# Kernel tuning notes

Measured on AMD Instinct MI355X. Metric: run time of the kernel, lower is better.

The kernel has to match this reference:

```python
import jax, jax.numpy as jnp
import numpy as np

NEG_INF = -1e18  # fp32 masking constant used by the original module


def setup_inputs() -> dict:
    key0 = jax.random.key(0)
    kq, kk, kv, km, ke = jax.random.split(key0, 5)
    B, L, H, C = 2, 2048, 16, 64
    query = jax.random.normal(kq, (B, L, H, C), dtype=jnp.float32)
    key = jax.random.normal(kk, (B, L, H, C), dtype=jnp.float32)
    value = jax.random.normal(kv, (B, L, H, C), dtype=jnp.float32)
    mask = jax.random.randint(km, (B, L, L), 0, 2).astype(jnp.bool_)
    edge_scores = jax.random.normal(ke, (1, H, L, L), dtype=jnp.float32)
    return {"query": query, "key": key, "value": value, "mask": mask,
            "edge_scores": edge_scores}


def _masked_softmax(att_score, mask):
    # mask: True -> keep, False -> masked. Fill with -1e18 (fp32 path),
    # softmax, then multiply by mask (post-softmax zeroing), as in original.
    s = jnp.where(mask, att_score, NEG_INF)
    w = jax.nn.softmax(s, axis=-1)
    return w * mask.astype(w.dtype)


def reference(query, key, value, mask, edge_scores):
    # layout 'NTK': query/key/value (B, L, H, C); mask (B, Lq, Lm)
    scale = jnp.sqrt(jnp.asarray(query.shape[-1], dtype=query.dtype))
    # scores: (B, H, Lq, Lm)
    scores = jnp.einsum('binc,bjnc->bnij', query, key)
    scores = scores + edge_scores
    attn_weights = _masked_softmax(scores / scale, mask[:, None, :, :])
    # dropout rate is 0.0 -> identity
    # context: (B, Lq, H, Cv) -> (B, Lq, H*Cv)
    context = jnp.einsum('bnij,bjnc->binc', attn_weights, value)
    B, Lq = context.shape[0], context.shape[1]
    context_vec = context.reshape(B, Lq, -1)
    return (context_vec, scores, attn_weights)
```

## Files before the change

kernel.cpp:

```cpp
#include <hip/hip_runtime.h>


typedef __attribute__((ext_vector_type(8))) short bf16x8;
typedef __attribute__((ext_vector_type(4))) float f32x4;

#define LQ 2048
#define NH 16
#define CD 64

__device__ inline short f2bf(float x) {
    union { float f; unsigned u; } v; v.f = x;
    unsigned r = v.u + 0x7FFFu + ((v.u >> 16) & 1u);
    return (short)(r >> 16);
}

__device__ inline bf16x8 pack8(float4 a, float4 b) {
    bf16x8 r;
    r[0] = f2bf(a.x); r[1] = f2bf(a.y); r[2] = f2bf(a.z); r[3] = f2bf(a.w);
    r[4] = f2bf(b.x); r[5] = f2bf(b.y); r[6] = f2bf(b.z); r[7] = f2bf(b.w);
    return r;
}

__global__ __launch_bounds__(256)
void k_stats(const float* __restrict__ q, const float* __restrict__ kk,
             const float* __restrict__ edge, const int* __restrict__ mask,
             float* __restrict__ lsum)
{
    __shared__ short Ks[64][72];
    __shared__ float Sf[4][16][68];
    const int z = blockIdx.y;
    const int b = z & 1, h = z >> 1;
    const int i0 = blockIdx.x * 64;
    const int tid = threadIdx.x;
    const int r = tid >> 2, seg = (tid & 3) * 16;
    const int wave = tid >> 6, lane = tid & 63;
    const int quad = lane >> 4, mm = lane & 15;

    const float* qp = q + ((size_t)((b * LQ + i0 + wave * 16 + mm) * NH + h)) * CD;
    float4 q0 = *(const float4*)(qp + quad * 8);
    float4 q1 = *(const float4*)(qp + quad * 8 + 4);
    float4 q2 = *(const float4*)(qp + 32 + quad * 8);
    float4 q3 = *(const float4*)(qp + 32 + quad * 8 + 4);
    bf16x8 a0 = pack8(q0, q1), a1 = pack8(q2, q3);

    float lacc[4] = {0.f, 0.f, 0.f, 0.f};

    for (int jb = 0; jb < 32; ++jb) {
        const int j0 = jb * 64;
        __syncthreads();
        const float* krow = kk + ((size_t)((b * LQ + j0 + r) * NH + h)) * CD + seg;
        #pragma unroll
        for (int u = 0; u < 4; ++u) {
            float4 g = ((const float4*)krow)[u];
            *(short4*)&Ks[r][seg + u * 4] = make_short4(f2bf(g.x), f2bf(g.y), f2bf(g.z), f2bf(g.w));
        }
        __syncthreads();

        #pragma unroll
        for (int jt = 0; jt < 4; ++jt) {
            bf16x8 b0 = *(const bf16x8*)&Ks[jt * 16 + mm][quad * 8];
            bf16x8 b1 = *(const bf16x8*)&Ks[jt * 16 + mm][32 + quad * 8];
            f32x4 a = {0.f, 0.f, 0.f, 0.f};
            a = __builtin_amdgcn_mfma_f32_16x16x32_bf16(a0, b0, a, 0, 0, 0);
            a = __builtin_amdgcn_mfma_f32_16x16x32_bf16(a1, b1, a, 0, 0, 0);
            #pragma unroll
            for (int reg = 0; reg < 4; ++reg)
                Sf[wave][quad * 4 + reg][jt * 16 + mm] = a[reg];
        }

        #pragma unroll
        for (int s = 0; s < 4; ++s) {
            const int rl = quad + 4 * s;
            const int gi = i0 + wave * 16 + rl;
            const int gj = j0 + mm * 4;
            float4 sv = *(const float4*)&Sf[wave][rl][mm * 4];
            float4 ev = *(const float4*)(edge + ((size_t)(h * LQ + gi)) * LQ + gj);
            int4   mv = *(const int4*)(mask + ((size_t)(b * LQ + gi)) * LQ + gj);
            float p0 = mv.x ? __expf((sv.x + ev.x) * 0.125f) : 0.f;
            float p1 = mv.y ? __expf((sv.y + ev.y) * 0.125f) : 0.f;
            float p2 = mv.z ? __expf((sv.z + ev.z) * 0.125f) : 0.f;
            float p3 = mv.w ? __expf((sv.w + ev.w) * 0.125f) : 0.f;
            lacc[s] += (p0 + p1) + (p2 + p3);
        }
    }

    #pragma unroll
    for (int s = 0; s < 4; ++s) {
        float v = lacc[s];
        #pragma unroll
        for (int o = 1; o <= 8; o <<= 1) v += __shfl_xor(v, o, 64);
        if (mm == 0)
            lsum[(size_t)(b * NH + h) * LQ + i0 + wave * 16 + quad + 4 * s] = v;
    }
}

__global__ __launch_bounds__(256)
void k_fused(const float* __restrict__ q, const float* __restrict__ kk,
             const float* __restrict__ v, const int* __restrict__ mask,
             const float* __restrict__ edge, const float* __restrict__ lsum,
             float* __restrict__ sc, float* __restrict__ attn,
             float* __restrict__ ctx)
{
    __shared__ short Ks[64][72];
    __shared__ short Vt[64][72];
    __shared__ float Sf[4][16][68];
    __shared__ short Wt[4][16][72];

    const int z = blockIdx.y;
    const int b = z & 1, h = z >> 1;
    const int i0 = blockIdx.x * 64;
    const int tid = threadIdx.x;
    const int r = tid >> 2, seg = (tid & 3) * 16;
    const int wave = tid >> 6, lane = tid & 63;
    const int quad = lane >> 4, mm = lane & 15;

    const float* qp = q + ((size_t)((b * LQ + i0 + wave * 16 + mm) * NH + h)) * CD;
    float4 q0 = *(const float4*)(qp + quad * 8);
    float4 q1 = *(const float4*)(qp + quad * 8 + 4);
    float4 q2 = *(const float4*)(qp + 32 + quad * 8);
    float4 q3 = *(const float4*)(qp + 32 + quad * 8 + 4);
    bf16x8 a0 = pack8(q0, q1), a1 = pack8(q2, q3);

    float inv[4];
    #pragma unroll
    for (int s = 0; s < 4; ++s) {
        float l = lsum[(size_t)(b * NH + h) * LQ + i0 + wave * 16 + quad + 4 * s];
        inv[s] = (l > 0.f) ? 1.f / l : 0.f;
    }

    f32x4 cacc[4] = { {0,0,0,0}, {0,0,0,0}, {0,0,0,0}, {0,0,0,0} };

    for (int jb = 0; jb < 32; ++jb) {
        const int j0 = jb * 64;
        __syncthreads();
        const float* krow = kk + ((size_t)((b * LQ + j0 + r) * NH + h)) * CD + seg;
        const float* vrow = v  + ((size_t)((b * LQ + j0 + r) * NH + h)) * CD + seg;
        #pragma unroll
        for (int u = 0; u < 4; ++u) {
            float4 g = ((const float4*)krow)[u];
            *(short4*)&Ks[r][seg + u * 4] = make_short4(f2bf(g.x), f2bf(g.y), f2bf(g.z), f2bf(g.w));
            float4 w = ((const float4*)vrow)[u];
            Vt[seg + u * 4 + 0][r] = f2bf(w.x);
            Vt[seg + u * 4 + 1][r] = f2bf(w.y);
            Vt[seg + u * 4 + 2][r] = f2bf(w.z);
            Vt[seg + u * 4 + 3][r] = f2bf(w.w);
        }
        __syncthreads();

        #pragma unroll
        for (int jt = 0; jt < 4; ++jt) {
            bf16x8 b0 = *(const bf16x8*)&Ks[jt * 16 + mm][quad * 8];
            bf16x8 b1 = *(const bf16x8*)&Ks[jt * 16 + mm][32 + quad * 8];
            f32x4 a = {0.f, 0.f, 0.f, 0.f};
            a = __builtin_amdgcn_mfma_f32_16x16x32_bf16(a0, b0, a, 0, 0, 0);
            a = __builtin_amdgcn_mfma_f32_16x16x32_bf16(a1, b1, a, 0, 0, 0);
            #pragma unroll
            for (int reg = 0; reg < 4; ++reg)
                Sf[wave][quad * 4 + reg][jt * 16 + mm] = a[reg];
        }

        #pragma unroll
        for (int s = 0; s < 4; ++s) {
            const int rl = quad + 4 * s;
            const int gi = i0 + wave * 16 + rl;
            const int gj = j0 + mm * 4;
            float4 sv = *(const float4*)&Sf[wave][rl][mm * 4];
            float4 ev = *(const float4*)(edge + ((size_t)(h * LQ + gi)) * LQ + gj);
            float4 s4 = make_float4(sv.x + ev.x, sv.y + ev.y, sv.z + ev.z, sv.w + ev.w);
            const size_t sidx = ((size_t)((b * NH + h) * LQ + gi)) * LQ + gj;
            *(float4*)(sc + sidx) = s4;
            int4 mv = *(const int4*)(mask + ((size_t)(b * LQ + gi)) * LQ + gj);
            const float iv = inv[s];
            float w0 = mv.x ? __expf(s4.x * 0.125f) * iv : 0.f;
            float w1 = mv.y ? __expf(s4.y * 0.125f) * iv : 0.f;
            float w2 = mv.z ? __expf(s4.z * 0.125f) * iv : 0.f;
            float w3 = mv.w ? __expf(s4.w * 0.125f) * iv : 0.f;
            *(float4*)(attn + sidx) = make_float4(w0, w1, w2, w3);
            *(short4*)&Wt[wave][rl][mm * 4] = make_short4(f2bf(w0), f2bf(w1), f2bf(w2), f2bf(w3));
        }

        #pragma unroll
        for (int kt = 0; kt < 2; ++kt) {
            bf16x8 aw = *(const bf16x8*)&Wt[wave][mm][kt * 32 + quad * 8];
            #pragma unroll
            for (int nt = 0; nt < 4; ++nt) {
                bf16x8 bb = *(const bf16x8*)&Vt[nt * 16 + mm][kt * 32 + quad * 8];
                cacc[nt] = __builtin_amdgcn_mfma_f32_16x16x32_bf16(aw, bb, cacc[nt], 0, 0, 0);
            }
        }
    }

    const int irow = i0 + wave * 16 + quad * 4;
    #pragma unroll
    for (int nt = 0; nt < 4; ++nt) {
        const int c = nt * 16 + mm;
        #pragma unroll
        for (int reg = 0; reg < 4; ++reg) {
            const int i = irow + reg;
            ctx[((size_t)(b * LQ + i)) * (NH * CD) + h * CD + c] = cacc[nt][reg];
        }
    }
}

extern "C" void kernel_launch(void* const* d_in, const int* in_sizes, int n_in,
                              void* d_out, int out_size, void* d_ws, size_t ws_size,
                              hipStream_t stream) {
    const float* q    = (const float*)d_in[0];
    const float* k    = (const float*)d_in[1];
    const float* v    = (const float*)d_in[2];
    const int*   mask = (const int*)d_in[3];
    const float* edge = (const float*)d_in[4];

    float* out = (float*)d_out;
    float* ctx = out;
    float* sc  = out + 4194304;
    float* at  = sc + 134217728;

    float* lsum = (float*)d_ws;

    k_stats<<<dim3(32, 32), 256, 0, stream>>>(q, k, edge, mask, lsum);
    k_fused<<<dim3(32, 32), 256, 0, stream>>>(q, k, v, mask, edge, lsum, sc, at, ctx);
}
```

Before: 1.795 ms.

## Swap MFMA operands to drop LDS score staging and prefetch edge/mask tiles

Both kernels now compute S^T via swapped MFMA operands, so each lane holds four consecutive key columns of one query row in registers. This removes the Sf shared-memory round trip and its extra LDS traffic. Edge and mask values for the next key block are loaded into registers one iteration early to hide global latency. Launch bounds now request 4 blocks per CU, which may force register spills given the added prefetch registers.

```diff
diff --git a/kernel.cpp b/kernel.cpp
--- a/kernel.cpp
+++ b/kernel.cpp
@@ -21,13 +21,12 @@
     return r;
 }
 
-__global__ __launch_bounds__(256)
+__global__ __launch_bounds__(256, 4)
 void k_stats(const float* __restrict__ q, const float* __restrict__ kk,
              const float* __restrict__ edge, const int* __restrict__ mask,
              float* __restrict__ lsum)
 {
     __shared__ short Ks[64][72];
-    __shared__ float Sf[4][16][68];
     const int z = blockIdx.y;
     const int b = z & 1, h = z >> 1;
     const int i0 = blockIdx.x * 64;
@@ -36,14 +35,22 @@
     const int wave = tid >> 6, lane = tid & 63;
     const int quad = lane >> 4, mm = lane & 15;
 
-    const float* qp = q + ((size_t)((b * LQ + i0 + wave * 16 + mm) * NH + h)) * CD;
-    float4 q0 = *(const float4*)(qp + quad * 8);
-    float4 q1 = *(const float4*)(qp + quad * 8 + 4);
-    float4 q2 = *(const float4*)(qp + 32 + quad * 8);
-    float4 q3 = *(const float4*)(qp + 32 + quad * 8 + 4);
-    bf16x8 a0 = pack8(q0, q1), a1 = pack8(q2, q3);
-
-    float lacc[4] = {0.f, 0.f, 0.f, 0.f};
+    const int gi = i0 + wave * 16 + mm;
+    const float* qp = q + ((size_t)((b * LQ + gi) * NH + h)) * CD;
+    bf16x8 qa0 = pack8(*(const float4*)(qp + quad * 8), *(const float4*)(qp + quad * 8 + 4));
+    bf16x8 qa1 = pack8(*(const float4*)(qp + 32 + quad * 8), *(const float4*)(qp + 32 + quad * 8 + 4));
+
+    const float* erow = edge + ((size_t)(h * LQ + gi)) * LQ;
+    const int*   mrow = mask + ((size_t)(b * LQ + gi)) * LQ;
+
+    float4 ev[4]; int4 mv[4];
+    #pragma unroll
+    for (int jt = 0; jt < 4; ++jt) {
+        ev[jt] = *(const float4*)(erow + jt * 16 + quad * 4);
+        mv[jt] = *(const int4*)(mrow + jt * 16 + quad * 4);
+    }
+
+    float lacc = 0.f;
 
     for (int jb = 0; jb < 32; ++jb) {
         const int j0 = jb * 64;
@@ -56,45 +63,42 @@
         }
         __syncthreads();
 
-        #pragma unroll
-        for (int jt = 0; jt < 4; ++jt) {
-            bf16x8 b0 = *(const bf16x8*)&Ks[jt * 16 + mm][quad * 8];
-            bf16x8 b1 = *(const bf16x8*)&Ks[jt * 16 + mm][32 + quad * 8];
+        f32x4 acc[4];
+        #pragma unroll
+        for (int jt = 0; jt < 4; ++jt) {
+            bf16x8 k0 = *(const bf16x8*)&Ks[jt * 16 + mm][quad * 8];
+            bf16x8 k1 = *(const bf16x8*)&Ks[jt * 16 + mm][32 + quad * 8];
             f32x4 a = {0.f, 0.f, 0.f, 0.f};
-            a = __builtin_amdgcn_mfma_f32_16x16x32_bf16(a0, b0, a, 0, 0, 0);
-            a = __builtin_amdgcn_mfma_f32_16x16x32_bf16(a1, b1, a, 0, 0, 0);
+            a = __builtin_amdgcn_mfma_f32_16x16x32_bf16(k0, qa0, a, 0, 0, 0);
+            a = __builtin_amdgcn_mfma_f32_16x16x32_bf16(k1, qa1, a, 0, 0, 0);
+            acc[jt] = a;
+        }
+
+        #pragma unroll
+        for (int jt = 0; jt < 4; ++jt) {
+            float p0 = mv[jt].x ? __expf((acc[jt][0] + ev[jt].x) * 0.125f) : 0.f;
+            float p1 = mv[jt].y ? __expf((acc[jt][1] + ev[jt].y) * 0.125f) : 0.f;
+            float p2 = mv[jt].z ? __expf((acc[jt][2] + ev[jt].z) * 0.125f) : 0.f;
+            float p3 = mv[jt].w ? __expf((acc[jt][3] + ev[jt].w) * 0.125f) : 0.f;
+            lacc += (p0 + p1) + (p2 + p3);
+        }
+
+        if (jb < 31) {
             #pragma unroll
-            for (int reg = 0; reg < 4; ++reg)
-                Sf[wave][quad * 4 + reg][jt * 16 + mm] = a[reg];
-        }
-
-        #pragma unroll
-        for (int s = 0; s < 4; ++s) {
-            const int rl = quad + 4 * s;
-            const int gi = i0 + wave * 16 + rl;
-            const int gj = j0 + mm * 4;
-            float4 sv = *(const float4*)&Sf[wave][rl][mm * 4];
-            float4 ev = *(const float4*)(edge + ((size_t)(h * LQ + gi)) * LQ + gj);
-            int4   mv = *(const int4*)(mask + ((size_t)(b * LQ + gi)) * LQ + gj);
-            float p0 = mv.x ? __expf((sv.x + ev.x) * 0.125f) : 0.f;
-            float p1 = mv.y ? __expf((sv.y + ev.y) * 0.125f) : 0.f;
-            float p2 = mv.z ? __expf((sv.z + ev.z) * 0.125f) : 0.f;
-            float p3 = mv.w ? __expf((sv.w + ev.w) * 0.125f) : 0.f;
-            lacc[s] += (p0 + p1) + (p2 + p3);
-        }
-    }
-
-    #pragma unroll
-    for (int s = 0; s < 4; ++s) {
-        float v = lacc[s];
-        #pragma unroll
-        for (int o = 1; o <= 8; o <<= 1) v += __shfl_xor(v, o, 64);
-        if (mm == 0)
-            lsum[(size_t)(b * NH + h) * LQ + i0 + wave * 16 + quad + 4 * s] = v;
-    }
-}
-
-__global__ __launch_bounds__(256)
+            for (int jt = 0; jt < 4; ++jt) {
+                ev[jt] = *(const float4*)(erow + j0 + 64 + jt * 16 + quad * 4);
+                mv[jt] = *(const int4*)(mrow + j0 + 64 + jt * 16 + quad * 4);
+            }
+        }
+    }
+
+    lacc += __shfl_xor(lacc, 16, 64);
+    lacc += __shfl_xor(lacc, 32, 64);
+    if (quad == 0)
+        lsum[(size_t)(b * NH + h) * LQ + gi] = lacc;
+}
+
+__global__ __launch_bounds__(256, 4)
 void k_fused(const float* __restrict__ q, const float* __restrict__ kk,
              const float* __restrict__ v, const int* __restrict__ mask,
              const float* __restrict__ edge, const float* __restrict__ lsum,
@@ -103,7 +107,6 @@
 {
     __shared__ short Ks[64][72];
     __shared__ short Vt[64][72];
-    __shared__ float Sf[4][16][68];
     __shared__ short Wt[4][16][72];
 
     const int z = blockIdx.y;
@@ -114,18 +117,23 @@
     const int wave = tid >> 6, lane = tid & 63;
     const int quad = lane >> 4, mm = lane & 15;
 
-    const float* qp = q + ((size_t)((b * LQ + i0 + wave * 16 + mm) * NH + h)) * CD;
-    float4 q0 = *(const float4*)(qp + quad * 8);
-    float4 q1 = *(const float4*)(qp + quad * 8 + 4);
-    float4 q2 = *(const float4*)(qp + 32 + quad * 8);
-    float4 q3 = *(const float4*)(qp + 32 + quad * 8 + 4);
-    bf16x8 a0 = pack8(q0, q1), a1 = pack8(q2, q3);
-
-    float inv[4];
+    const int gi = i0 + wave * 16 + mm;
+    const float* qp = q + ((size_t)((b * LQ + gi) * NH + h)) * CD;
+    bf16x8 qa0 = pack8(*(const float4*)(qp + quad * 8), *(const float4*)(qp + quad * 8 + 4));
+    bf16x8 qa1 = pack8(*(const float4*)(qp + 32 + quad * 8), *(const float4*)(qp + 32 + quad * 8 + 4));
+
+    const float* erow = edge + ((size_t)(h * LQ + gi)) * LQ;
+    const int*   mrow = mask + ((size_t)(b * LQ + gi)) * LQ;
+    const size_t srow = ((size_t)((b * NH + h) * LQ + gi)) * LQ;
+
+    const float l = lsum[(size_t)(b * NH + h) * LQ + gi];
+    const float inv = (l > 0.f) ? 1.f / l : 0.f;
+
+    float4 ev[4]; int4 mv[4];
     #pragma unroll
-    for (int s = 0; s < 4; ++s) {
-        float l = lsum[(size_t)(b * NH + h) * LQ + i0 + wave * 16 + quad + 4 * s];
-        inv[s] = (l > 0.f) ? 1.f / l : 0.f;
+    for (int jt = 0; jt < 4; ++jt) {
+        ev[jt] = *(const float4*)(erow + jt * 16 + quad * 4);
+        mv[jt] = *(const int4*)(mrow + jt * 16 + quad * 4);
     }
 
     f32x4 cacc[4] = { {0,0,0,0}, {0,0,0,0}, {0,0,0,0}, {0,0,0,0} };
@@ -147,36 +155,37 @@
         }
         __syncthreads();
 
-        #pragma unroll
-        for (int jt = 0; jt < 4; ++jt) {
-            bf16x8 b0 = *(const bf16x8*)&Ks[jt * 16 + mm][quad * 8];
-            bf16x8 b1 = *(const bf16x8*)&Ks[jt * 16 + mm][32 + quad * 8];
+        f32x4 acc[4];
+        #pragma unroll
+        for (int jt = 0; jt < 4; ++jt) {
+            bf16x8 k0 = *(const bf16x8*)&Ks[jt * 16 + mm][quad * 8];
+            bf16x8 k1 = *(const bf16x8*)&Ks[jt * 16 + mm][32 + quad * 8];
             f32x4 a = {0.f, 0.f, 0.f, 0.f};
-            a = __builtin_amdgcn_mfma_f32_16x16x32_bf16(a0, b0, a, 0, 0, 0);
-            a = __builtin_amdgcn_mfma_f32_16x16x32_bf16(a1, b1, a, 0, 0, 0);
+            a = __builtin_amdgcn_mfma_f32_16x16x32_bf16(k0, qa0, a, 0, 0, 0);
+            a = __builtin_amdgcn_mfma_f32_16x16x32_bf16(k1, qa1, a, 0, 0, 0);
+            acc[jt] = a;
+        }
+
+        #pragma unroll
+        for (int jt = 0; jt < 4; ++jt) {
+            const int jl = jt * 16 + quad * 4;
+            float4 s4 = make_float4(acc[jt][0] + ev[jt].x, acc[jt][1] + ev[jt].y,
+                                    acc[jt][2] + ev[jt].z, acc[jt][3] + ev[jt].w);
+            *(float4*)(sc + srow + j0 + jl) = s4;
+            float w0 = mv[jt].x ? __expf(s4.x * 0.125f) * inv : 0.f;
+            float w1 = mv[jt].y ? __expf(s4.y * 0.125f) * inv : 0.f;
+            float w2 = mv[jt].z ? __expf(s4.z * 0.125f) * inv : 0.f;
+            float w3 = mv[jt].w ? __expf(s4.w * 0.125f) * inv : 0.f;
+            *(float4*)(attn + srow + j0 + jl) = make_float4(w0, w1, w2, w3);
+            *(short4*)&Wt[wave][mm][jl] = make_short4(f2bf(w0), f2bf(w1), f2bf(w2), f2bf(w3));
+        }
+
+        if (jb < 31) {
             #pragma unroll
-            for (int reg = 0; reg < 4; ++reg)
-                Sf[wave][quad * 4 + reg][jt * 16 + mm] = a[reg];
-        }
-
-        #pragma unroll
-        for (int s = 0; s < 4; ++s) {
-            const int rl = quad + 4 * s;
-            const int gi = i0 + wave * 16 + rl;
-            const int gj = j0 + mm * 4;
-            float4 sv = *(const float4*)&Sf[wave][rl][mm * 4];
-            float4 ev = *(const float4*)(edge + ((size_t)(h * LQ + gi)) * LQ + gj);
-            float4 s4 = make_float4(sv.x + ev.x, sv.y + ev.y, sv.z + ev.z, sv.w + ev.w);
-            const size_t sidx = ((size_t)((b * NH + h) * LQ + gi)) * LQ + gj;
-            *(float4*)(sc + sidx) = s4;
-            int4 mv = *(const int4*)(mask + ((size_t)(b * LQ + gi)) * LQ + gj);
-            const float iv = inv[s];
-            float w0 = mv.x ? __expf(s4.x * 0.125f) * iv : 0.f;
-            float w1 = mv.y ? __expf(s4.y * 0.125f) * iv : 0.f;
-            float w2 = mv.z ? __expf(s4.z * 0.125f) * iv : 0.f;
-            float w3 = mv.w ? __expf(s4.w * 0.125f) * iv : 0.f;
-            *(float4*)(attn + sidx) = make_float4(w0, w1, w2, w3);
-            *(short4*)&Wt[wave][rl][mm * 4] = make_short4(f2bf(w0), f2bf(w1), f2bf(w2), f2bf(w3));
+            for (int jt = 0; jt < 4; ++jt) {
+                ev[jt] = *(const float4*)(erow + j0 + 64 + jt * 16 + quad * 4);
+                mv[jt] = *(const int4*)(mrow + j0 + 64 + jt * 16 + quad * 4);
+            }
         }
 
         #pragma unroll
```

Measured after the change: 1.653 ms. 1.09x faster.
